# Performance work log

Measured on AMD Instinct MI355X. Metric: run time of the kernel, lower is better.

The kernel has to match this reference:

```python
import jax, jax.numpy as jnp
import numpy as np

D_MODEL = 1024
NUM_HEADS = 16
DEPTH = D_MODEL // NUM_HEADS
B, S = 2, 2048


def setup_inputs() -> dict:
    key = jax.random.key(0)
    k1, k2, k3 = jax.random.split(key, 3)
    x = jax.random.normal(k1, (B, S, D_MODEL), dtype=jnp.float32)
    # causal mask: 1.0 where attention is disallowed (upper triangle)
    causal = 1.0 - jnp.tril(jnp.ones((S, S), dtype=jnp.float32))
    mask = causal[None, None, :, :]  # [1,1,S,S]
    w_attn = jax.random.normal(k2, (D_MODEL, 3 * D_MODEL), dtype=jnp.float32) * 0.02
    b_attn = jnp.zeros((3 * D_MODEL,), dtype=jnp.float32)
    w_proj = jax.random.normal(k3, (D_MODEL, D_MODEL), dtype=jnp.float32) * 0.02
    b_proj = jnp.zeros((D_MODEL,), dtype=jnp.float32)
    return {"x": x, "mask": mask, "w_attn": w_attn, "b_attn": b_attn,
            "w_proj": w_proj, "b_proj": b_proj}


def _split_heads(t):
    # [B,S,D] -> [B,H,S,depth]
    b, s, _ = t.shape
    return t.reshape(b, s, NUM_HEADS, DEPTH).transpose(0, 2, 1, 3)


def reference(x, mask, w_attn, b_attn, w_proj, b_proj):
    # QKV projection (Conv1d == pointwise dense over last axis)
    qkv = jnp.einsum('bsd,de->bse', x, w_attn) + b_attn
    q, k, v = jnp.split(qkv, 3, axis=2)
    q, k, v = _split_heads(q), _split_heads(k), _split_heads(v)  # [B,H,S,depth]
    present = jnp.stack([k, v], axis=1)  # [B,2,H,S,depth]
    # scaled dot-product attention (inference: no dropout)
    scores = jnp.einsum('bhqd,bhkd->bhqk', q, k) / jnp.sqrt(
        jnp.asarray(DEPTH, dtype=x.dtype))
    scores = scores + mask * (-1e9)
    attn = jax.nn.softmax(scores, axis=-1)
    out = jnp.einsum('bhqk,bhkd->bhqd', attn, v)
    # merge heads: [B,H,S,depth] -> [B,S,D]
    out = out.transpose(0, 2, 1, 3).reshape(x.shape[0], -1, D_MODEL)
    out = jnp.einsum('bsd,de->bse', out, w_proj) + b_proj
    return out, present
```

## Files before the change

### kernel.cpp

```cpp
#include <hip/hip_runtime.h>
#include <stdint.h>

typedef unsigned short u16;
typedef unsigned int u32;
typedef short bf16x8 __attribute__((ext_vector_type(8)));
typedef float f32x4 __attribute__((ext_vector_type(4)));
typedef float f32x16 __attribute__((ext_vector_type(16)));

#define SEQ 2048
#define NH 16
#define DM 1024
#define DEPTH 64

#define QSCALE 0.18033688f
#define SMAX 16.0f

__device__ __forceinline__ u16 f2bf(float f) {
  union { float f; u32 i; } v; v.f = f;
  u32 x = v.i;
  x += 0x7fffu + ((x >> 16) & 1u);
  return (u16)(x >> 16);
}

__device__ __forceinline__ float fexp2(float x) {
#if __has_builtin(__builtin_amdgcn_exp2f)
  return __builtin_amdgcn_exp2f(x);
#else
  return exp2f(x);
#endif
}

__device__ __forceinline__ u32 cvtpk(float lo, float hi) {
  u32 r;
  asm("v_cvt_pk_bf16_f32 %0, %1, %2" : "=v"(r) : "v"(lo), "v"(hi));
  return r;
}
__device__ __forceinline__ float bflo(u32 w) {
  union { u32 i; float f; } u; u.i = w << 16; return u.f;
}
__device__ __forceinline__ float bfhi(u32 w) {
  union { u32 i; float f; } u; u.i = w & 0xffff0000u; return u.f;
}

__device__ __forceinline__ void gload_lds16(const u16* g, u16* l) {
  __builtin_amdgcn_global_load_lds(
      (const __attribute__((address_space(1))) u32*)g,
      (__attribute__((address_space(3))) u32*)l, 16, 0, 0);
}

__global__ __launch_bounds__(256)
void cvt_bf16(const float* __restrict__ src, u16* __restrict__ dst) {
  int i = (blockIdx.x * 256 + threadIdx.x) * 4;
  float4 v = *(const float4*)(src + i);
  ushort4 o; o.x = f2bf(v.x); o.y = f2bf(v.y); o.z = f2bf(v.z); o.w = f2bf(v.w);
  *(ushort4*)(dst + i) = o;
}

__global__ __launch_bounds__(256)
void cvtT_both(const float* __restrict__ wa, const float* __restrict__ wp,
               u16* __restrict__ dwa, u16* __restrict__ dwp) {
  __shared__ float t[32][33];
  const int tid = threadIdx.x;
  const int bx = blockIdx.x;
  const float* src; u16* dst; int N, n0;
  if (bx < 96) { src = wa; dst = dwa; N = 3 * DM; n0 = bx << 5; }
  else         { src = wp; dst = dwp; N = DM;     n0 = (bx - 96) << 5; }
  const int k0 = blockIdx.y << 5;
  const int K = DM;
  {
    int r = tid >> 3, c4 = (tid & 7) << 2;
    float4 v = *(const float4*)(src + (size_t)(k0 + r) * N + n0 + c4);
    t[r][c4 + 0] = v.x; t[r][c4 + 1] = v.y; t[r][c4 + 2] = v.z; t[r][c4 + 3] = v.w;
  }
  __syncthreads();
  {
    int n = tid >> 3, k4 = (tid & 7) << 2;
    ushort4 o;
    o.x = f2bf(t[k4 + 0][n]); o.y = f2bf(t[k4 + 1][n]);
    o.z = f2bf(t[k4 + 2][n]); o.w = f2bf(t[k4 + 3][n]);
    *(ushort4*)(dst + (size_t)(n0 + n) * K + k0 + k4) = o;
  }
}

__global__ __launch_bounds__(256)
void v_transpose(const float* __restrict__ present, u16* __restrict__ vt) {
  __shared__ float t[64][65];
  const int tid = threadIdx.x;
  const int st = blockIdx.x, bh = blockIdx.y;
  const int b = bh >> 4, h = bh & 15;
  const int s0 = st << 6;
  const float* vsrc = present + (((size_t)((b * 2 + 1) * NH + h)) * SEQ + s0) * DEPTH;
  u16* vdst = vt + ((size_t)(b * NH + h) * DEPTH) * SEQ + s0;
#pragma unroll
  for (int i = 0; i < 4; ++i) {
    int e = tid + (i << 8);
    int r = e >> 4, c = e & 15;
    float4 v = *(const float4*)(vsrc + (size_t)r * DEPTH + (c << 2));
    t[r][(c << 2) + 0] = v.x; t[r][(c << 2) + 1] = v.y;
    t[r][(c << 2) + 2] = v.z; t[r][(c << 2) + 3] = v.w;
  }
  __syncthreads();
#pragma unroll
  for (int i = 0; i < 2; ++i) {
    int e = tid + (i << 8);
    int d = e >> 3, s8 = (e & 7) << 3;
    ushort4 o0, o1;
    o0.x = f2bf(t[s8 + 0][d]); o0.y = f2bf(t[s8 + 1][d]);
    o0.z = f2bf(t[s8 + 2][d]); o0.w = f2bf(t[s8 + 3][d]);
    o1.x = f2bf(t[s8 + 4][d]); o1.y = f2bf(t[s8 + 5][d]);
    o1.z = f2bf(t[s8 + 6][d]); o1.w = f2bf(t[s8 + 7][d]);
    *(ushort4*)(vdst + (size_t)d * SEQ + s8) = o0;
    *(ushort4*)(vdst + (size_t)d * SEQ + s8 + 4) = o1;
  }
}

__global__ __launch_bounds__(256)
void gemm_mfma(const u16* __restrict__ A, const u16* __restrict__ Bt,
               const float* __restrict__ bias, int M, int N, int K, int mode,
               float* __restrict__ outf, u16* __restrict__ qws,
               float* __restrict__ present, u16* __restrict__ kbp)
{
  __shared__ __align__(16) u16 As[2][128][64];
  __shared__ __align__(16) u16 Bs[2][128][64];
  const int tid = threadIdx.x;

  const u32 nwg = gridDim.x * gridDim.y;
  const u32 bid0 = blockIdx.y * gridDim.x + blockIdx.x;
  const u32 cpx = nwg >> 3;
  const u32 bid = (bid0 & 7) * cpx + (bid0 >> 3);
  const int m0 = (int)(bid / gridDim.x) << 7;
  const int n0 = (int)(bid % gridDim.x) << 7;

  const int w = tid >> 6, lane = tid & 63;
  const int lane15 = lane & 15, quad = lane >> 4;
  const int wm = (w >> 1) << 6, wn = (w & 1) << 6;

  const int srow = lane >> 3;
  const int sseg = (lane & 7) ^ srow;
  const u16* agbase = A  + (size_t)(m0 + w * 32 + srow) * K + sseg * 8;
  const u16* bgbase = Bt + (size_t)(n0 + w * 32 + srow) * K + sseg * 8;

  const int l7 = lane15 & 7;

  f32x4 acc[4][4] = {};

  const int nk = K >> 6;
#pragma unroll
  for (int i = 0; i < 4; ++i) {
    gload_lds16(agbase + (size_t)(i * 8) * K, &As[0][w * 32 + i * 8][0]);
    gload_lds16(bgbase + (size_t)(i * 8) * K, &Bs[0][w * 32 + i * 8][0]);
  }
  __syncthreads();

#pragma unroll 1
  for (int kt = 0; kt < nk; ++kt) {
    const int cur = kt & 1;
    if (kt + 1 < nk) {
      const int kn = (kt + 1) << 6;
#pragma unroll
      for (int i = 0; i < 4; ++i) {
        gload_lds16(agbase + (size_t)(i * 8) * K + kn, &As[cur ^ 1][w * 32 + i * 8][0]);
        gload_lds16(bgbase + (size_t)(i * 8) * K + kn, &Bs[cur ^ 1][w * 32 + i * 8][0]);
      }
    }
#pragma unroll
    for (int ks = 0; ks < 2; ++ks) {
      const int fs = ((ks * 4 + quad) ^ l7) << 3;
      bf16x8 af[4], bfr[4];
#pragma unroll
      for (int tm = 0; tm < 4; ++tm)
        af[tm] = *(const bf16x8*)&As[cur][wm + tm * 16 + lane15][fs];
#pragma unroll
      for (int tn = 0; tn < 4; ++tn)
        bfr[tn] = *(const bf16x8*)&Bs[cur][wn + tn * 16 + lane15][fs];
      __builtin_amdgcn_s_setprio(1);
#pragma unroll
      for (int tm = 0; tm < 4; ++tm)
#pragma unroll
        for (int tn = 0; tn < 4; ++tn)
          acc[tm][tn] = __builtin_amdgcn_mfma_f32_16x16x32_bf16(af[tm], bfr[tn], acc[tm][tn], 0, 0, 0);
      __builtin_amdgcn_s_setprio(0);
    }
    __syncthreads();
  }

#pragma unroll
  for (int tn = 0; tn < 4; ++tn) {
    const int c = n0 + wn + tn * 16 + lane15;
    const float bc = bias[c];
    const int t = c >> 10, cc = c & 1023;
    const int h = cc >> 6, d = cc & 63;
#pragma unroll
    for (int tm = 0; tm < 4; ++tm) {
#pragma unroll
      for (int r = 0; r < 4; ++r) {
        const int m = m0 + wm + tm * 16 + quad * 4 + r;
        const float val = acc[tm][tn][r] + bc;
        if (mode == 1) {
          outf[(size_t)m * N + c] = val;
        } else {
          const int b = m >> 11, s = m & 2047;
          if (t == 0) {
            qws[(((size_t)(b * NH + h) * SEQ) + s) * DEPTH + d] = f2bf(val * QSCALE);
          } else {
            const size_t pidx = (((size_t)((b * 2 + (t - 1)) * NH + h) * SEQ) + s) * DEPTH + d;
            present[pidx] = val;
            if (t == 1)
              kbp[(((size_t)(b * NH + h) * SEQ) + s) * DEPTH + d] = f2bf(val);
          }
        }
      }
    }
  }
}

__global__ __launch_bounds__(256, 4)
void attn_mfma(const u16* __restrict__ qb, const u16* __restrict__ kb,
               const u16* __restrict__ vt, u16* __restrict__ attnb)
{
  __shared__ __align__(16) u16 Ks[2][64][64];
  __shared__ __align__(16) u16 Vs[2][64][64];

  const int tid = threadIdx.x;
  const int w = tid >> 6, lane = tid & 63;
  const int l31 = lane & 31, hi = lane >> 5;
  const int qh = w >> 1, kh = w & 1;
  const int tt = blockIdx.x, bh = blockIdx.y;
  const int b = bh >> 4, h = bh & 15;

  const u16* qbh = qb + ((size_t)(b * NH + h) * SEQ) * DEPTH;
  const u16* kbh = kb + ((size_t)(b * NH + h) * SEQ) * DEPTH;
  const u16* vbh = vt + ((size_t)(b * NH + h) * DEPTH) * SEQ;

  const int srr = lane >> 3;
  const int sseg = (lane & 7) ^ srr;
  const int r0 = w * 16 + srr;
  const int r1 = r0 + 8;
  const int kr0 = (r0 & ~12) | ((r0 & 4) << 1) | ((r0 & 8) >> 1);
  const int kr1 = (r1 & ~12) | ((r1 & 4) << 1) | ((r1 & 8) >> 1);

  const int rbase = kh * 32 + l31;
  const int swz = l31 & 7;

  const int sloc = (tt << 6) + qh * 32 + l31;
  const int nch = tt + 1;

  const int koff0 = ((0 + hi) ^ swz) << 4;
  const int koff1 = ((2 + hi) ^ swz) << 4;
  const int koff2 = ((4 + hi) ^ swz) << 4;
  const int koff3 = ((6 + hi) ^ swz) << 4;
  const int voffA = ((kh * 4 + 0 + hi) ^ swz) << 4;
  const int voffB = ((kh * 4 + 2 + hi) ^ swz) << 4;

  const u16* kgp0 = kbh + (size_t)kr0 * DEPTH + sseg * 8;
  const u16* kgp1 = kbh + (size_t)kr1 * DEPTH + sseg * 8;
  const u16* vgp0 = vbh + (size_t)r0 * SEQ + sseg * 8;
  const u16* vgp1 = vbh + (size_t)r1 * SEQ + sseg * 8;

  gload_lds16(kgp0, &Ks[0][w * 16][0]);
  gload_lds16(kgp1, &Ks[0][w * 16 + 8][0]);
  gload_lds16(vgp0, &Vs[0][w * 16][0]);
  gload_lds16(vgp1, &Vs[0][w * 16 + 8][0]);

  const u16* qrow = qbh + (size_t)sloc * DEPTH + hi * 8;
  bf16x8 qf0 = *(const bf16x8*)(qrow);
  bf16x8 qf1 = *(const bf16x8*)(qrow + 16);
  bf16x8 qf2 = *(const bf16x8*)(qrow + 32);
  bf16x8 qf3 = *(const bf16x8*)(qrow + 48);

  f32x16 accO0 = {};
  f32x16 accO1 = {};
  float L = 0.f;

  __syncthreads();

#pragma unroll 1
  for (int ct = 0; ct < nch; ++ct) {
    const int bb = ct & 1;
    if (ct + 1 < nch) {
      kgp0 += 64 * DEPTH; kgp1 += 64 * DEPTH;
      vgp0 += 64; vgp1 += 64;
      gload_lds16(kgp0, &Ks[bb ^ 1][w * 16][0]);
      gload_lds16(kgp1, &Ks[bb ^ 1][w * 16 + 8][0]);
      gload_lds16(vgp0, &Vs[bb ^ 1][w * 16][0]);
      gload_lds16(vgp1, &Vs[bb ^ 1][w * 16 + 8][0]);
    }
    const bool atdiag = (ct == tt);
    if (!(atdiag && qh == 0 && kh == 1)) {
      const char* kbase = (const char*)&Ks[bb][rbase][0];
      f32x16 sc;
#pragma unroll
      for (int j = 0; j < 16; ++j) sc[j] = -SMAX;
      {
        bf16x8 af0 = *(const bf16x8*)(kbase + koff0);
        sc = __builtin_amdgcn_mfma_f32_32x32x16_bf16(af0, qf0, sc, 0, 0, 0);
        bf16x8 af1 = *(const bf16x8*)(kbase + koff1);
        sc = __builtin_amdgcn_mfma_f32_32x32x16_bf16(af1, qf1, sc, 0, 0, 0);
        bf16x8 af2 = *(const bf16x8*)(kbase + koff2);
        sc = __builtin_amdgcn_mfma_f32_32x32x16_bf16(af2, qf2, sc, 0, 0, 0);
        bf16x8 af3 = *(const bf16x8*)(kbase + koff3);
        sc = __builtin_amdgcn_mfma_f32_32x32x16_bf16(af3, qf3, sc, 0, 0, 0);
      }
      float pe[16];
      if (atdiag && (qh == kh)) {
#pragma unroll
        for (int j = 0; j < 16; ++j) {
          float e = fexp2(sc[j]);
          if ((16 * (j >> 3) + 8 * hi + (j & 7)) > l31) e = 0.f;
          pe[j] = e;
        }
      } else {
#pragma unroll
        for (int j = 0; j < 16; ++j) pe[j] = fexp2(sc[j]);
      }
      const u32 pk0 = cvtpk(pe[0], pe[1]),   pk1 = cvtpk(pe[2], pe[3]);
      const u32 pk2 = cvtpk(pe[4], pe[5]),   pk3 = cvtpk(pe[6], pe[7]);
      const u32 pk4 = cvtpk(pe[8], pe[9]),   pk5 = cvtpk(pe[10], pe[11]);
      const u32 pk6 = cvtpk(pe[12], pe[13]), pk7 = cvtpk(pe[14], pe[15]);
      float l0 = bflo(pk0) + bfhi(pk0);
      float l1 = bflo(pk1) + bfhi(pk1);
      l0 += bflo(pk2) + bfhi(pk2);
      l1 += bflo(pk3) + bfhi(pk3);
      l0 += bflo(pk4) + bfhi(pk4);
      l1 += bflo(pk5) + bfhi(pk5);
      l0 += bflo(pk6) + bfhi(pk6);
      l1 += bflo(pk7) + bfhi(pk7);
      L += l0 + l1;
      union { u32 u[4]; bf16x8 v; } f0, f1;
      f0.u[0] = pk0; f0.u[1] = pk1; f0.u[2] = pk2; f0.u[3] = pk3;
      f1.u[0] = pk4; f1.u[1] = pk5; f1.u[2] = pk6; f1.u[3] = pk7;
      const char* vbase = (const char*)&Vs[bb][l31][0];
      {
        bf16x8 av0 = *(const bf16x8*)(vbase + voffA);
        accO0 = __builtin_amdgcn_mfma_f32_32x32x16_bf16(av0, f0.v, accO0, 0, 0, 0);
        bf16x8 av1 = *(const bf16x8*)(vbase + 4096 + voffA);
        accO1 = __builtin_amdgcn_mfma_f32_32x32x16_bf16(av1, f0.v, accO1, 0, 0, 0);
        bf16x8 av2 = *(const bf16x8*)(vbase + voffB);
        accO0 = __builtin_amdgcn_mfma_f32_32x32x16_bf16(av2, f1.v, accO0, 0, 0, 0);
        bf16x8 av3 = *(const bf16x8*)(vbase + 4096 + voffB);
        accO1 = __builtin_amdgcn_mfma_f32_32x32x16_bf16(av3, f1.v, accO1, 0, 0, 0);
      }
    }
    __syncthreads();
  }

  float Lw = L + __shfl_xor(L, 32);
  float* red  = (float*)&Ks[0][0][0];
  float* redL = (float*)&Vs[0][0][0];
  const int base = qh * 2048 + lane * 4;
  if (kh) {
#pragma unroll
    for (int g = 0; g < 4; ++g) {
      float4 v0 = make_float4(accO0[4 * g], accO0[4 * g + 1], accO0[4 * g + 2], accO0[4 * g + 3]);
      *(float4*)&red[base + g * 256] = v0;
      float4 v1 = make_float4(accO1[4 * g], accO1[4 * g + 1], accO1[4 * g + 2], accO1[4 * g + 3]);
      *(float4*)&red[base + 1024 + g * 256] = v1;
    }
    redL[qh * 64 + lane] = Lw;
  }
  __syncthreads();
  if (!kh) {
    const float li = 1.0f / (Lw + redL[qh * 64 + lane]);
    u16* ob = attnb + ((size_t)(b * SEQ + sloc)) * DM + h * DEPTH;
#pragma unroll
    for (int g = 0; g < 4; ++g) {
      float4 p0 = *(const float4*)&red[base + g * 256];
      ushort4 st0;
      st0.x = f2bf((accO0[4 * g + 0] + p0.x) * li);
      st0.y = f2bf((accO0[4 * g + 1] + p0.y) * li);
      st0.z = f2bf((accO0[4 * g + 2] + p0.z) * li);
      st0.w = f2bf((accO0[4 * g + 3] + p0.w) * li);
      *(ushort4*)(ob + 8 * g + 4 * hi) = st0;
      float4 p1 = *(const float4*)&red[base + 1024 + g * 256];
      ushort4 st1;
      st1.x = f2bf((accO1[4 * g + 0] + p1.x) * li);
      st1.y = f2bf((accO1[4 * g + 1] + p1.y) * li);
      st1.z = f2bf((accO1[4 * g + 2] + p1.z) * li);
      st1.w = f2bf((accO1[4 * g + 3] + p1.w) * li);
      *(ushort4*)(ob + 32 + 8 * g + 4 * hi) = st1;
    }
  }
}

extern "C" void kernel_launch(void* const* d_in, const int* in_sizes, int n_in,
                              void* d_out, int out_size, void* d_ws, size_t ws_size,
                              hipStream_t stream) {
  (void)in_sizes; (void)n_in; (void)out_size; (void)ws_size;
  const float* x      = (const float*)d_in[0];
  const float* w_attn = (const float*)d_in[2];
  const float* b_attn = (const float*)d_in[3];
  const float* w_proj = (const float*)d_in[4];
  const float* b_proj = (const float*)d_in[5];

  float* out     = (float*)d_out;
  float* present = out + (size_t)2 * SEQ * DM;

  u16* qws   = (u16*)d_ws;
  u16* kbp   = qws + (size_t)4194304;
  u16* xb    = kbp + (size_t)4194304;
  u16* vtp   = xb;
  u16* wabT  = xb + (size_t)4194304;
  u16* attnb = wabT;
  u16* wpbT  = wabT + (size_t)4194304;

  cvt_bf16<<<4096, 256, 0, stream>>>(x, xb);
  cvtT_both<<<dim3(128, 32), 256, 0, stream>>>(w_attn, w_proj, wabT, wpbT);

  gemm_mfma<<<dim3(24, 32), 256, 0, stream>>>(xb, wabT, b_attn,
                                              2 * SEQ, 3 * DM, DM, 0,
                                              nullptr, qws, present, kbp);
  v_transpose<<<dim3(32, 32), 256, 0, stream>>>(present, vtp);
  attn_mfma<<<dim3(32, 32), 256, 0, stream>>>(qws, kbp, vtp, attnb);
  gemm_mfma<<<dim3(8, 32), 256, 0, stream>>>(attnb, wpbT, b_proj,
                                             2 * SEQ, DM, DM, 1,
                                             out, nullptr, nullptr, nullptr);
}
```

Before: 222.5 us.

## Fuse conversion kernels, halve GEMM M-tile, write V-transpose in GEMM epilogue, rotate attention tiles

Merges the x conversion and the weight transpose-conversion into one launch. Shrinks the GEMM M tile from 128 to 64 rows so each GEMM launches twice as many workgroups. When the workspace is large enough, the QKV GEMM epilogue writes the transposed bf16 V directly, so the separate v_transpose kernel is skipped. Attention block indices are rotated so causal work of different sizes is spread across the grid. The epilogue V writes are strided by SEQ and uncoalesced, and the smaller tile lowers arithmetic intensity.

```diff
diff --git a/kernel.cpp b/kernel.cpp
--- a/kernel.cpp
+++ b/kernel.cpp
@@ -49,23 +49,25 @@
 }
 
 __global__ __launch_bounds__(256)
-void cvt_bf16(const float* __restrict__ src, u16* __restrict__ dst) {
-  int i = (blockIdx.x * 256 + threadIdx.x) * 4;
-  float4 v = *(const float4*)(src + i);
-  ushort4 o; o.x = f2bf(v.x); o.y = f2bf(v.y); o.z = f2bf(v.z); o.w = f2bf(v.w);
-  *(ushort4*)(dst + i) = o;
-}
-
-__global__ __launch_bounds__(256)
-void cvtT_both(const float* __restrict__ wa, const float* __restrict__ wp,
+void cvt_fused(const float* __restrict__ x, u16* __restrict__ xb,
+               const float* __restrict__ wa, const float* __restrict__ wp,
                u16* __restrict__ dwa, u16* __restrict__ dwp) {
   __shared__ float t[32][33];
   const int tid = threadIdx.x;
-  const int bx = blockIdx.x;
+  int bx = blockIdx.x;
+  if (bx < 4096) {
+    int i = (bx * 256 + tid) * 4;
+    float4 v = *(const float4*)(x + i);
+    ushort4 o; o.x = f2bf(v.x); o.y = f2bf(v.y); o.z = f2bf(v.z); o.w = f2bf(v.w);
+    *(ushort4*)(xb + i) = o;
+    return;
+  }
+  bx -= 4096;
+  const int cx = bx & 127, cy = bx >> 7;
   const float* src; u16* dst; int N, n0;
-  if (bx < 96) { src = wa; dst = dwa; N = 3 * DM; n0 = bx << 5; }
-  else         { src = wp; dst = dwp; N = DM;     n0 = (bx - 96) << 5; }
-  const int k0 = blockIdx.y << 5;
+  if (cx < 96) { src = wa; dst = dwa; N = 3 * DM; n0 = cx << 5; }
+  else         { src = wp; dst = dwp; N = DM;     n0 = (cx - 96) << 5; }
+  const int k0 = cy << 5;
   const int K = DM;
   {
     int r = tid >> 3, c4 = (tid & 7) << 2;
@@ -118,9 +120,10 @@
 void gemm_mfma(const u16* __restrict__ A, const u16* __restrict__ Bt,
                const float* __restrict__ bias, int M, int N, int K, int mode,
                float* __restrict__ outf, u16* __restrict__ qws,
-               float* __restrict__ present, u16* __restrict__ kbp)
+               float* __restrict__ present, u16* __restrict__ kbp,
+               u16* __restrict__ vtp)
 {
-  __shared__ __align__(16) u16 As[2][128][64];
+  __shared__ __align__(16) u16 As[2][64][64];
   __shared__ __align__(16) u16 Bs[2][128][64];
   const int tid = threadIdx.x;
 
@@ -128,28 +131,29 @@
   const u32 bid0 = blockIdx.y * gridDim.x + blockIdx.x;
   const u32 cpx = nwg >> 3;
   const u32 bid = (bid0 & 7) * cpx + (bid0 >> 3);
-  const int m0 = (int)(bid / gridDim.x) << 7;
+  const int m0 = (int)(bid / gridDim.x) << 6;
   const int n0 = (int)(bid % gridDim.x) << 7;
 
   const int w = tid >> 6, lane = tid & 63;
   const int lane15 = lane & 15, quad = lane >> 4;
-  const int wm = (w >> 1) << 6, wn = (w & 1) << 6;
+  const int wm = (w >> 1) << 5, wn = (w & 1) << 6;
 
   const int srow = lane >> 3;
   const int sseg = (lane & 7) ^ srow;
-  const u16* agbase = A  + (size_t)(m0 + w * 32 + srow) * K + sseg * 8;
+  const u16* agbase = A  + (size_t)(m0 + w * 16 + srow) * K + sseg * 8;
   const u16* bgbase = Bt + (size_t)(n0 + w * 32 + srow) * K + sseg * 8;
 
   const int l7 = lane15 & 7;
 
-  f32x4 acc[4][4] = {};
+  f32x4 acc[2][4] = {};
 
   const int nk = K >> 6;
 #pragma unroll
-  for (int i = 0; i < 4; ++i) {
-    gload_lds16(agbase + (size_t)(i * 8) * K, &As[0][w * 32 + i * 8][0]);
+  for (int i = 0; i < 2; ++i)
+    gload_lds16(agbase + (size_t)(i * 8) * K, &As[0][w * 16 + i * 8][0]);
+#pragma unroll
+  for (int i = 0; i < 4; ++i)
     gload_lds16(bgbase + (size_t)(i * 8) * K, &Bs[0][w * 32 + i * 8][0]);
-  }
   __syncthreads();
 
 #pragma unroll 1
@@ -158,24 +162,25 @@
     if (kt + 1 < nk) {
       const int kn = (kt + 1) << 6;
 #pragma unroll
-      for (int i = 0; i < 4; ++i) {
-        gload_lds16(agbase + (size_t)(i * 8) * K + kn, &As[cur ^ 1][w * 32 + i * 8][0]);
+      for (int i = 0; i < 2; ++i)
+        gload_lds16(agbase + (size_t)(i * 8) * K + kn, &As[cur ^ 1][w * 16 + i * 8][0]);
+#pragma unroll
+      for (int i = 0; i < 4; ++i)
         gload_lds16(bgbase + (size_t)(i * 8) * K + kn, &Bs[cur ^ 1][w * 32 + i * 8][0]);
-      }
     }
 #pragma unroll
     for (int ks = 0; ks < 2; ++ks) {
       const int fs = ((ks * 4 + quad) ^ l7) << 3;
-      bf16x8 af[4], bfr[4];
-#pragma unroll
-      for (int tm = 0; tm < 4; ++tm)
+      bf16x8 af[2], bfr[4];
+#pragma unroll
+      for (int tm = 0; tm < 2; ++tm)
         af[tm] = *(const bf16x8*)&As[cur][wm + tm * 16 + lane15][fs];
 #pragma unroll
       for (int tn = 0; tn < 4; ++tn)
         bfr[tn] = *(const bf16x8*)&Bs[cur][wn + tn * 16 + lane15][fs];
       __builtin_amdgcn_s_setprio(1);
 #pragma unroll
-      for (int tm = 0; tm < 4; ++tm)
+      for (int tm = 0; tm < 2; ++tm)
 #pragma unroll
         for (int tn = 0; tn < 4; ++tn)
           acc[tm][tn] = __builtin_amdgcn_mfma_f32_16x16x32_bf16(af[tm], bfr[tn], acc[tm][tn], 0, 0, 0);
@@ -191,7 +196,7 @@
     const int t = c >> 10, cc = c & 1023;
     const int h = cc >> 6, d = cc & 63;
 #pragma unroll
-    for (int tm = 0; tm < 4; ++tm) {
+    for (int tm = 0; tm < 2; ++tm) {
 #pragma unroll
       for (int r = 0; r < 4; ++r) {
         const int m = m0 + wm + tm * 16 + quad * 4 + r;
@@ -207,6 +212,8 @@
             present[pidx] = val;
             if (t == 1)
               kbp[(((size_t)(b * NH + h) * SEQ) + s) * DEPTH + d] = f2bf(val);
+            else if (vtp)
+              vtp[((size_t)(b * NH + h) * DEPTH + d) * SEQ + s] = f2bf(val);
           }
         }
       }
@@ -225,7 +232,8 @@
   const int w = tid >> 6, lane = tid & 63;
   const int l31 = lane & 31, hi = lane >> 5;
   const int qh = w >> 1, kh = w & 1;
-  const int tt = blockIdx.x, bh = blockIdx.y;
+  const int bh = blockIdx.y;
+  const int tt = (blockIdx.x + blockIdx.y) & 31;
   const int b = bh >> 4, h = bh & 15;
 
   const u16* qbh = qb + ((size_t)(b * NH + h) * SEQ) * DEPTH;
@@ -385,7 +393,7 @@
 extern "C" void kernel_launch(void* const* d_in, const int* in_sizes, int n_in,
                               void* d_out, int out_size, void* d_ws, size_t ws_size,
                               hipStream_t stream) {
-  (void)in_sizes; (void)n_in; (void)out_size; (void)ws_size;
+  (void)in_sizes; (void)n_in; (void)out_size;
   const float* x      = (const float*)d_in[0];
   const float* w_attn = (const float*)d_in[2];
   const float* b_attn = (const float*)d_in[3];
@@ -398,20 +406,22 @@
   u16* qws   = (u16*)d_ws;
   u16* kbp   = qws + (size_t)4194304;
   u16* xb    = kbp + (size_t)4194304;
-  u16* vtp   = xb;
   u16* wabT  = xb + (size_t)4194304;
-  u16* attnb = wabT;
   u16* wpbT  = wabT + (size_t)4194304;
-
-  cvt_bf16<<<4096, 256, 0, stream>>>(x, xb);
-  cvtT_both<<<dim3(128, 32), 256, 0, stream>>>(w_attn, w_proj, wabT, wpbT);
-
-  gemm_mfma<<<dim3(24, 32), 256, 0, stream>>>(xb, wabT, b_attn,
+  const bool fused = ws_size >= (size_t)21 * 1024 * 1024 * 2 * 2;
+  u16* vtp   = fused ? (wpbT + (size_t)1048576) : xb;
+  u16* attnb = fused ? xb : wabT;
+
+  cvt_fused<<<8192, 256, 0, stream>>>(x, xb, w_attn, w_proj, wabT, wpbT);
+
+  gemm_mfma<<<dim3(24, 64), 256, 0, stream>>>(xb, wabT, b_attn,
                                               2 * SEQ, 3 * DM, DM, 0,
-                                              nullptr, qws, present, kbp);
-  v_transpose<<<dim3(32, 32), 256, 0, stream>>>(present, vtp);
+                                              nullptr, qws, present, kbp,
+                                              fused ? vtp : nullptr);
+  if (!fused)
+    v_transpose<<<dim3(32, 32), 256, 0, stream>>>(present, vtp);
   attn_mfma<<<dim3(32, 32), 256, 0, stream>>>(qws, kbp, vtp, attnb);
-  gemm_mfma<<<dim3(8, 32), 256, 0, stream>>>(attnb, wpbT, b_proj,
+  gemm_mfma<<<dim3(8, 64), 256, 0, stream>>>(attnb, wpbT, b_proj,
                                              2 * SEQ, DM, DM, 1,
-                                             out, nullptr, nullptr, nullptr);
-}
+                                             out, nullptr, nullptr, nullptr, nullptr);
+}
```

New measurement: 205.5 us. 7.6% less time.
